# Kernel tuning notes

Measured on AMD Instinct MI355X. Metric: run time of the kernel, lower is better.

Reference implementation:

```python
import jax, jax.numpy as jnp
import numpy as np

B, L, HID = 2, 2048, 2560
H, HKV, DH = 32, 8, 128
G = H // HKV  # GQA groups = 4
EPS = 1e-6
THETA = 1000000.0


def setup_inputs() -> dict:
    key = jax.random.key(0)
    ks = jax.random.split(key, 6)
    x = jax.random.normal(ks[0], (B, L, HID), dtype=jnp.float32)
    Wq = jax.random.normal(ks[1], (HID, H * DH), dtype=jnp.float32) * 0.02
    Wk = jax.random.normal(ks[2], (HID, HKV * DH), dtype=jnp.float32) * 0.02
    Wv = jax.random.normal(ks[3], (HID, HKV * DH), dtype=jnp.float32) * 0.02
    Wo = jax.random.normal(ks[4], (H * DH, HID), dtype=jnp.float32) * 0.02
    q_norm_w = jnp.ones((DH,), dtype=jnp.float32)
    k_norm_w = jnp.ones((DH,), dtype=jnp.float32)
    # RoPE tables, theta=1e6, non-interleaved (half-split) layout
    inv_freq = 1.0 / (THETA ** (jnp.arange(0, DH, 2, dtype=jnp.float32) / DH))
    pos = jnp.arange(L, dtype=jnp.float32)
    freqs = pos[:, None] * inv_freq[None, :]              # [L, DH/2]
    emb = jnp.concatenate([freqs, freqs], axis=-1)        # [L, DH]
    cos = jnp.broadcast_to(jnp.cos(emb)[None], (B, L, DH))
    sin = jnp.broadcast_to(jnp.sin(emb)[None], (B, L, DH))
    return {"x": x, "Wq": Wq, "Wk": Wk, "Wv": Wv, "Wo": Wo,
            "q_norm_w": q_norm_w, "k_norm_w": k_norm_w,
            "cos": cos, "sin": sin}


def _rmsnorm(x, w):
    xf = x.astype(jnp.float32)
    var = jnp.mean(xf * xf, axis=-1, keepdims=True)
    return (xf * jax.lax.rsqrt(var + EPS)).astype(x.dtype) * w


def _rotate_half(x):
    x1, x2 = jnp.split(x, 2, axis=-1)
    return jnp.concatenate([-x2, x1], axis=-1)


def reference(x, Wq, Wk, Wv, Wo, q_norm_w, k_norm_w, cos, sin):
    b, l, _ = x.shape
    q = (x @ Wq).reshape(b, l, H, DH)
    k = (x @ Wk).reshape(b, l, HKV, DH)
    v = (x @ Wv).reshape(b, l, HKV, DH).transpose(0, 2, 1, 3)   # [B,HKV,L,DH]
    q = _rmsnorm(q, q_norm_w).transpose(0, 2, 1, 3)             # [B,H,L,DH]
    k = _rmsnorm(k, k_norm_w).transpose(0, 2, 1, 3)             # [B,HKV,L,DH]
    c = cos[:, None]  # [B,1,L,DH]
    s = sin[:, None]
    q = q * c + _rotate_half(q) * s
    k = k * c + _rotate_half(k) * s
    # GQA SDPA, causal
    qg = q.reshape(b, HKV, G, l, DH)
    scale = 1.0 / np.sqrt(DH)
    scores = jnp.einsum('bkgqd,bkmd->bkgqm', qg, k) * scale     # [B,HKV,G,L,L]
    causal = jnp.tril(jnp.ones((l, l), dtype=bool))
    scores = jnp.where(causal, scores, jnp.finfo(scores.dtype).min)
    attn = jax.nn.softmax(scores, axis=-1)
    out = jnp.einsum('bkgqm,bkmd->bkgqd', attn, v)              # [B,HKV,G,L,DH]
    out = out.reshape(b, H, l, DH).transpose(0, 2, 1, 3).reshape(b, l, H * DH)
    return out @ Wo
```

## Files before the change

### kernel.cpp

```cpp
#include <hip/hip_runtime.h>

typedef unsigned short u16;
typedef unsigned int u32;
using bf16x8 = __attribute__((ext_vector_type(8))) __bf16;
using f32x4  = __attribute__((ext_vector_type(4))) float;

typedef const void __attribute__((address_space(1)))* gas1p;
typedef void __attribute__((address_space(3)))* las3p;

__device__ __forceinline__ void gload16(const void* g, void* l) {
  __builtin_amdgcn_global_load_lds((gas1p)g, (las3p)l, 16, 0, 0);
}

__device__ __forceinline__ u16 f2bf(float f) {
  union { float f; unsigned u; } v; v.f = f;
  unsigned r = v.u + 0x7FFFu + ((v.u >> 16) & 1u);
  return (u16)(r >> 16);
}
__device__ __forceinline__ float bf2f(u16 h) {
  union { unsigned u; float f; } v; v.u = ((unsigned)h) << 16;
  return v.f;
}

__global__ __launch_bounds__(256)
void cvt_f32_bf16(const float4* __restrict__ in, uint2* __restrict__ out, int n4) {
  int i = blockIdx.x * 256 + threadIdx.x;
  if (i >= n4) return;
  float4 v = in[i];
  uint2 o;
  o.x = (unsigned)f2bf(v.x) | ((unsigned)f2bf(v.y) << 16);
  o.y = (unsigned)f2bf(v.z) | ((unsigned)f2bf(v.w) << 16);
  out[i] = o;
}

__global__ __launch_bounds__(256)
void transpose_w(const float* __restrict__ in, u16* __restrict__ out, int R, int C) {
  __shared__ float tile[32][33];
  const int tx = threadIdx.x & 31, ty = threadIdx.x >> 5;
  const int r0 = blockIdx.y * 32, c0 = blockIdx.x * 32;
#pragma unroll
  for (int i = 0; i < 4; i++)
    tile[ty + i * 8][tx] = in[(size_t)(r0 + ty + i * 8) * C + c0 + tx];
  __syncthreads();
#pragma unroll
  for (int i = 0; i < 4; i++)
    out[(size_t)(c0 + ty + i * 8) * R + r0 + tx] = f2bf(tile[tx][ty + i * 8]);
}

__global__ __launch_bounds__(256)
void transpose_v(const u16* __restrict__ QKV, u16* __restrict__ Vt) {
  __shared__ u16 tile[32][34];
  const int tx = threadIdx.x & 31, ty = threadIdx.x >> 5;
  const int l0 = blockIdx.x * 32, d0 = blockIdx.y * 32;
  const int bkv = blockIdx.z;
  const int b = bkv >> 3, kvh = bkv & 7;
#pragma unroll
  for (int i = 0; i < 4; i++)
    tile[ty + i * 8][tx] =
        QKV[(size_t)(b * 2048 + l0 + ty + i * 8) * 6144 + 5120 + kvh * 128 + d0 + tx];
  __syncthreads();
#pragma unroll
  for (int i = 0; i < 4; i++)
    Vt[((size_t)bkv * 128 + d0 + ty + i * 8) * 2048 + l0 + tx] = tile[tx][ty + i * 8];
}

__global__ __launch_bounds__(256)
void norm_rope(const u16* __restrict__ QKV, const float* __restrict__ qw,
               const float* __restrict__ kw, const float* __restrict__ cosp,
               const float* __restrict__ sinp, u16* __restrict__ Qr,
               u16* __restrict__ Kr) {
  const int rid = blockIdx.x * 4 + (threadIdx.x >> 6);
  const int lane = threadIdx.x & 63;
  const int head = rid % 40;
  const int bl = rid / 40;
  const int b = bl >> 11, l = bl & 2047;
  const u16* src; const float* w; u16* dst; float scale;
  if (head < 32) {
    src = QKV + (size_t)bl * 6144 + head * 128;
    w = qw;
    dst = Qr + ((size_t)(b * 32 + head) * 2048 + l) * 128;
    scale = 0.08838834764831845f;
  } else {
    const int kvh = head - 32;
    src = QKV + (size_t)bl * 6144 + 4096 + kvh * 128;
    w = kw;
    dst = Kr + ((size_t)(b * 8 + kvh) * 2048 + l) * 128;
    scale = 1.0f;
  }
  float lo = bf2f(src[lane]);
  float hi = bf2f(src[lane + 64]);
  float ss = lo * lo + hi * hi;
#pragma unroll
  for (int m = 1; m < 64; m <<= 1) ss += __shfl_xor(ss, m, 64);
  const float rstd = rsqrtf(ss * (1.0f / 128.0f) + 1e-6f) * scale;
  const float nlo = lo * rstd * w[lane];
  const float nhi = hi * rstd * w[lane + 64];
  const float* cb = cosp + (size_t)bl * 128;
  const float* sb = sinp + (size_t)bl * 128;
  dst[lane]      = f2bf(nlo * cb[lane]      - nhi * sb[lane]);
  dst[lane + 64] = f2bf(nhi * cb[lane + 64] + nlo * sb[lane + 64]);
}

#define BAR __builtin_amdgcn_s_barrier()
#define WLG { asm volatile("s_waitcnt lgkmcnt(0)" ::: "memory");            \
              __builtin_amdgcn_sched_barrier(0); }
#define WVMn(n) asm volatile("s_waitcnt vmcnt(" #n ")" ::: "memory")
#define SP1 __builtin_amdgcn_s_setprio(1)
#define SP0 __builtin_amdgcn_s_setprio(0)

template <int BM, int BN, int WM, int WN, typename CT>
__global__ __launch_bounds__(512, 2)
void gemmT(const u16* __restrict__ A, const u16* __restrict__ Bt,
           CT* __restrict__ C, int N, int K, int MT) {
  extern __shared__ char smem[];
  constexpr int ASZ = BM * 128;
  constexpr int BSZ = BN * 128;
  constexpr int MI = BM / WM / 16;
  constexpr int NJF = BN / WN / 16;
  const int tid = threadIdx.x, lane = tid & 63, wid = tid >> 6;
  const int wm = wid / WN, wn = wid % WN;
  const int fr = lane & 15, fq = lane >> 4;
  const int qx = (int)gridDim.x >> 3;
  const int wg = ((int)blockIdx.x & 7) * qx + ((int)blockIdx.x >> 3);
  const int bx = wg / MT, by = wg - bx * MT;
  const int m0 = by * BM, n0 = bx * BN;
  const u16* Ab = A + (size_t)m0 * K;
  const u16* Bb = Bt + (size_t)n0 * K;

#define ABUF(c) (smem + (c) * ASZ)
#define BBUF(c) (smem + 2 * ASZ + (c) * BSZ)

  f32x4 acc[MI][NJF];
#pragma unroll
  for (int i = 0; i < MI; i++)
#pragma unroll
    for (int j = 0; j < NJF; j++)
#pragma unroll
      for (int r = 0; r < 4; r++) acc[i][j][r] = 0.f;

  auto stage = [&](int c, int kk) {
#pragma unroll
    for (int l = 0; l < BM / 64; l++) {
      const int u = tid + 512 * l, row = u >> 3, ch = u & 7;
      gload16(Ab + (size_t)row * K + ((ch ^ (row & 7)) << 3) + kk,
              ABUF(c) + (u << 4));
    }
#pragma unroll
    for (int l = 0; l < BN / 64; l++) {
      const int u = tid + 512 * l, row = u >> 3, ch = u & 7;
      gload16(Bb + (size_t)row * K + ((ch ^ (row & 7)) << 3) + kk,
              BBUF(c) + (u << 4));
    }
    if constexpr ((BN % 64) != 0) {
      const int u = (BN / 64) * 512 + (tid & 255), row = u >> 3, ch = u & 7;
      gload16(Bb + (size_t)row * K + ((ch ^ (row & 7)) << 3) + kk,
              BBUF(c) + (u << 4));
    }
  };

  const int NT = K >> 6;
  stage(0, 0);
  stage(1, 64);
  WVMn(7);
  BAR;

  bf16x8 af[MI][2], bf[NJF][2];
  for (int t = 0; t < NT; t++) {
    const int c = t & 1;
#pragma unroll
    for (int i = 0; i < MI; i++) {
      const int row = (wm * MI + i) * 16 + fr;
#pragma unroll
      for (int ks = 0; ks < 2; ks++)
        af[i][ks] = *(const bf16x8*)(ABUF(c) + row * 128 +
                                     ((((ks << 2) + fq) ^ (row & 7)) << 4));
    }
#pragma unroll
    for (int j = 0; j < NJF; j++) {
      const int row = (j * WN + wn) * 16 + fr;
#pragma unroll
      for (int ks = 0; ks < 2; ks++)
        bf[j][ks] = *(const bf16x8*)(BBUF(c) + row * 128 +
                                     ((((ks << 2) + fq) ^ (row & 7)) << 4));
    }
    WLG;
    BAR;
    int t2 = t + 2; if (t2 >= NT) t2 -= NT;
    stage(c, t2 << 6);
    WVMn(7);
    SP1;
#pragma unroll
    for (int j = 0; j < NJF; j++)
#pragma unroll
      for (int i = 0; i < MI; i++) {
        acc[i][j] = __builtin_amdgcn_mfma_f32_16x16x32_bf16(af[i][0], bf[j][0],
                                                            acc[i][j], 0, 0, 0);
        acc[i][j] = __builtin_amdgcn_mfma_f32_16x16x32_bf16(af[i][1], bf[j][1],
                                                            acc[i][j], 0, 0, 0);
      }
    SP0;
    BAR;
  }
  WVMn(0);

#pragma unroll
  for (int i = 0; i < MI; i++) {
    const int row0 = m0 + (wm * MI + i) * 16 + fq * 4;
#pragma unroll
    for (int j = 0; j < NJF; j++) {
      const int col = n0 + (j * WN + wn) * 16 + fr;
#pragma unroll
      for (int r = 0; r < 4; r++) {
        const size_t idx = (size_t)(row0 + r) * N + col;
        if constexpr (sizeof(CT) == 2) C[idx] = f2bf(acc[i][j][r]);
        else C[idx] = acc[i][j][r];
      }
    }
  }
#undef ABUF
#undef BBUF
}

__global__ __launch_bounds__(256, 2)
void attn_fwd(const u16* __restrict__ Qr, const u16* __restrict__ Kr,
              const u16* __restrict__ Vt, u16* __restrict__ AO) {
  const int L = 2048, DH = 128;
  __shared__ u16 Ks[2][64 * 128];
  __shared__ u16 Vs[2][128 * 64];
  const int tid = threadIdx.x, lane = tid & 63, wid = tid >> 6;
  const int fr = lane & 15, fq = lane >> 4;
  const int j = blockIdx.x >> 4;
  const int grp = blockIdx.x & 15;
  const int kvh = grp >> 1, b = grp & 1;
  const int h = kvh * 4 + wid;

  const u16* Kbase = Kr + (size_t)(b * 8 + kvh) * L * DH;
  const u16* Vbase = Vt + (size_t)(b * 8 + kvh) * DH * L;

  int Dly[4], kOff[4], vOff[4];
#pragma unroll
  for (int p = 0; p < 4; p++) {
    const int D = (tid + p * 256) * 16;
    Dly[p] = D;
    const int kr = D >> 8, kc = ((D >> 4) & 15) ^ (kr & 7);
    kOff[p] = kr * 128 + kc * 8;
    const int vr = D >> 7, vc = ((D >> 4) & 7) ^ (vr & 7);
    vOff[p] = vr * 2048 + vc * 8;
  }

  const bool B5 = (lane & 32) != 0;
  const bool A4 = (lane & 16) != 0;

  auto stage = [&](int kt, int bufi) {
    const int k0 = kt * 64;
#pragma unroll
    for (int p = 0; p < 4; p++) {
      gload16(Kbase + (size_t)k0 * 128 + kOff[p], (char*)&Ks[bufi][0] + Dly[p]);
      gload16(Vbase + k0 + vOff[p], (char*)&Vs[bufi][0] + Dly[p]);
    }
  };

  for (int half = 0; half < 2; half++) {
    const int t = half ? 63 - j : j;
    const int nk = (t >> 1) + 1;

    bf16x8 qf[2][4];
#pragma unroll
    for (int g = 0; g < 2; g++) {
      const int qq = t * 32 + g * 16 + fr;
      const u16* qbase = Qr + ((size_t)(b * 32 + h) * L + qq) * DH + fq * 8;
#pragma unroll
      for (int dt = 0; dt < 4; dt++) qf[g][dt] = *(const bf16x8*)(qbase + dt * 32);
    }
    asm volatile("s_waitcnt vmcnt(0)" ::: "memory");

    f32x4 o[2][8];
#pragma unroll
    for (int g = 0; g < 2; g++)
#pragma unroll
      for (int d = 0; d < 8; d++)
#pragma unroll
        for (int r = 0; r < 4; r++) o[g][d][r] = 0.f;
    float mrow[2] = {-__builtin_huge_valf(), -__builtin_huge_valf()};
    float lrow[2] = {0.f, 0.f};

    __builtin_amdgcn_s_barrier();
    stage(0, 0);
    int cur = 0;

    for (int kt = 0; kt < nk; kt++) {
      if (kt + 1 < nk) {
        stage(kt + 1, cur ^ 1);
        asm volatile("s_waitcnt vmcnt(8)" ::: "memory");
      } else {
        asm volatile("s_waitcnt vmcnt(0)" ::: "memory");
      }
      __builtin_amdgcn_s_barrier();

      const u16* KsB = &Ks[cur][0];
      const u16* VsB = &Vs[cur][0];
      const int k0 = kt * 64;

      f32x4 s4[2][4];
#pragma unroll
      for (int g = 0; g < 2; g++)
#pragma unroll
        for (int ni = 0; ni < 4; ni++)
#pragma unroll
          for (int r = 0; r < 4; r++) s4[g][ni][r] = 0.f;
#pragma unroll
      for (int ni = 0; ni < 4; ni++) {
        const int krow = ni * 16 + fr;
        const int sw = (krow & 7) << 4;
#pragma unroll
        for (int dt = 0; dt < 4; dt++) {
          const int off = (krow * 256 + dt * 64 + fq * 16) ^ sw;
          bf16x8 kf = *(const bf16x8*)((const char*)KsB + off);
          s4[0][ni] = __builtin_amdgcn_mfma_f32_16x16x32_bf16(kf, qf[0][dt], s4[0][ni], 0, 0, 0);
          s4[1][ni] = __builtin_amdgcn_mfma_f32_16x16x32_bf16(kf, qf[1][dt], s4[1][ni], 0, 0, 0);
        }
      }

      if (kt == nk - 1) {
#pragma unroll
        for (int g = 0; g < 2; g++) {
          const int qq = t * 32 + g * 16 + fr;
#pragma unroll
          for (int ni = 0; ni < 4; ni++)
#pragma unroll
            for (int r = 0; r < 4; r++)
              if (k0 + ni * 16 + fq * 4 + r > qq) s4[g][ni][r] = -1e30f;
        }
      }

      bf16x8 pb[2][2];
#pragma unroll
      for (int g = 0; g < 2; g++) {
        float mt = s4[g][0][0];
#pragma unroll
        for (int ni = 0; ni < 4; ni++)
#pragma unroll
          for (int r = 0; r < 4; r++) mt = fmaxf(mt, s4[g][ni][r]);
        mt = fmaxf(mt, __shfl_xor(mt, 16, 64));
        mt = fmaxf(mt, __shfl_xor(mt, 32, 64));

        if (!__all(mt <= mrow[g] + 8.f)) {
          const float mn = fmaxf(mrow[g], mt);
          const float corr = exp2f((mrow[g] - mn) * 1.44269504f);
          mrow[g] = mn;
          lrow[g] *= corr;
#pragma unroll
          for (int d = 0; d < 8; d++)
#pragma unroll
            for (int r = 0; r < 4; r++) o[g][d][r] *= corr;
        }

        const float ml = mrow[g] * 1.44269504f;
        float rs = 0.f;
#pragma unroll
        for (int ni = 0; ni < 4; ni++)
#pragma unroll
          for (int r = 0; r < 4; r++) {
            const float pv = exp2f(fmaf(s4[g][ni][r], 1.44269504f, -ml));
            s4[g][ni][r] = pv;
            rs += pv;
          }
        rs += __shfl_xor(rs, 16, 64);
        rs += __shfl_xor(rs, 32, 64);
        lrow[g] += rs;

        u32 pk[4][2];
#pragma unroll
        for (int ni = 0; ni < 4; ni++) {
          pk[ni][0] = __builtin_amdgcn_perm(__float_as_uint(s4[g][ni][1]),
                                            __float_as_uint(s4[g][ni][0]), 0x07060302u);
          pk[ni][1] = __builtin_amdgcn_perm(__float_as_uint(s4[g][ni][3]),
                                            __float_as_uint(s4[g][ni][2]), 0x07060302u);
        }
#pragma unroll
        for (int ks = 0; ks < 2; ks++) {
          u32 r00 = pk[2 * ks + 0][0], r01 = pk[2 * ks + 0][1];
          u32 r10 = pk[2 * ks + 1][0], r11 = pk[2 * ks + 1][1];
          u32 e0 = __shfl_xor(B5 ? r00 : r10, 32, 64);
          u32 t00 = B5 ? e0 : r00, t10 = B5 ? r10 : e0;
          u32 e1 = __shfl_xor(B5 ? r01 : r11, 32, 64);
          u32 t01 = B5 ? e1 : r01, t11 = B5 ? r11 : e1;
          u32 e2 = __shfl_xor(A4 ? t00 : t10, 16, 64);
          u32 u00 = A4 ? e2 : t00, u10 = A4 ? t10 : e2;
          u32 e3 = __shfl_xor(A4 ? t01 : t11, 16, 64);
          u32 u01 = A4 ? e3 : t01, u11 = A4 ? t11 : e3;
          union { u32 u[4]; bf16x8 v; } pbv;
          pbv.u[0] = u00; pbv.u[1] = u01; pbv.u[2] = u10; pbv.u[3] = u11;
          pb[g][ks] = pbv.v;
        }
      }

#pragma unroll
      for (int d = 0; d < 8; d++) {
        const int vrow = d * 16 + fr;
        const int sw = (vrow & 7) << 4;
#pragma unroll
        for (int ks = 0; ks < 2; ks++) {
          const int off = (vrow * 128 + ks * 64 + fq * 16) ^ sw;
          bf16x8 vf = *(const bf16x8*)((const char*)VsB + off);
          o[0][d] = __builtin_amdgcn_mfma_f32_16x16x32_bf16(vf, pb[0][ks], o[0][d], 0, 0, 0);
          o[1][d] = __builtin_amdgcn_mfma_f32_16x16x32_bf16(vf, pb[1][ks], o[1][d], 0, 0, 0);
        }
      }
      __builtin_amdgcn_s_barrier();
      cur ^= 1;
    }

#pragma unroll
    for (int g = 0; g < 2; g++) {
      const float inv = 1.f / lrow[g];
      const int qq = t * 32 + g * 16 + fr;
      u16* obase = AO + ((size_t)b * L + qq) * 4096 + h * 128 + fq * 4;
#pragma unroll
      for (int d = 0; d < 8; d++) {
        uint2 w;
        w.x = (u32)f2bf(o[g][d][0] * inv) | ((u32)f2bf(o[g][d][1] * inv) << 16);
        w.y = (u32)f2bf(o[g][d][2] * inv) | ((u32)f2bf(o[g][d][3] * inv) << 16);
        *(uint2*)(obase + d * 16) = w;
      }
    }
  }
}

extern "C" void kernel_launch(void* const* d_in, const int* in_sizes, int n_in,
                              void* d_out, int out_size, void* d_ws, size_t ws_size,
                              hipStream_t stream) {
  const float* x    = (const float*)d_in[0];
  const float* Wq   = (const float*)d_in[1];
  const float* Wk   = (const float*)d_in[2];
  const float* Wv   = (const float*)d_in[3];
  const float* Wo   = (const float*)d_in[4];
  const float* qw   = (const float*)d_in[5];
  const float* kw   = (const float*)d_in[6];
  const float* cosp = (const float*)d_in[7];
  const float* sinp = (const float*)d_in[8];
  float* out = (float*)d_out;
  char* ws = (char*)d_ws;

  u16* xb    = (u16*)(ws);
  u16* WqkvT = (u16*)(ws + 20971520);
  u16* WoT   = (u16*)(ws + 52428800);
  u16* QKV   = (u16*)(ws + 73400320);
  u16* AO    = QKV;
  u16* Qrr   = (u16*)(ws + 123731968);
  u16* Krr   = (u16*)(ws + 157286400);
  u16* Vtt   = (u16*)(ws + 165675008);

  hipFuncSetAttribute(reinterpret_cast<const void*>(&gemmT<256, 192, 2, 4, u16>),
                      hipFuncAttributeMaxDynamicSharedMemorySize, 114688);
  hipFuncSetAttribute(reinterpret_cast<const void*>(&gemmT<256, 160, 4, 2, float>),
                      hipFuncAttributeMaxDynamicSharedMemorySize, 106496);

  cvt_f32_bf16<<<10240, 256, 0, stream>>>((const float4*)x, (uint2*)xb, 2621440);
  transpose_w<<<dim3(128, 80), 256, 0, stream>>>(Wq, WqkvT, 2560, 4096);
  transpose_w<<<dim3(32, 80), 256, 0, stream>>>(Wk, WqkvT + (size_t)4096 * 2560, 2560, 1024);
  transpose_w<<<dim3(32, 80), 256, 0, stream>>>(Wv, WqkvT + (size_t)5120 * 2560, 2560, 1024);
  transpose_w<<<dim3(80, 128), 256, 0, stream>>>(Wo, WoT, 4096, 2560);

  gemmT<256, 192, 2, 4, u16><<<512, 512, 114688, stream>>>(xb, WqkvT, QKV, 6144, 2560, 16);

  norm_rope<<<40960, 256, 0, stream>>>(QKV, qw, kw, cosp, sinp, Qrr, Krr);
  transpose_v<<<dim3(64, 4, 16), 256, 0, stream>>>(QKV, Vtt);

  attn_fwd<<<dim3(512), 256, 0, stream>>>(Qrr, Krr, Vtt, AO);

  gemmT<256, 160, 4, 2, float><<<256, 512, 106496, stream>>>(AO, WoT, out, 2560, 4096, 16);
}
```

Before: 406.7 us.

## Shrink attention KV tile to 32 and QKV GEMM tile to raise occupancy

Restructures the attention kernel to process one 32-row query tile per block with 32-key KV tiles. Blocks are launched longest-first in place of pairing tiles per block, and the grid doubles. The PV product switches to 16x16x16 MFMA so the probability fragment no longer needs the cross-lane shuffle transpose, and the V shared layout is reswizzled to match. The QKV projection GEMM uses a 128-row tile with 4 waves-per-SIMD occupancy and twice as many workgroups. Both changes aim to improve latency hiding and load balance, at the cost of more barriers per key and smaller MFMA instructions.

```diff
diff --git a/kernel.cpp b/kernel.cpp
--- a/kernel.cpp
+++ b/kernel.cpp
@@ -4,6 +4,7 @@
 typedef unsigned int u32;
 using bf16x8 = __attribute__((ext_vector_type(8))) __bf16;
 using f32x4  = __attribute__((ext_vector_type(4))) float;
+using short4v = __attribute__((ext_vector_type(4))) short;
 
 typedef const void __attribute__((address_space(1)))* gas1p;
 typedef void __attribute__((address_space(3)))* las3p;
@@ -108,8 +109,8 @@
 #define SP1 __builtin_amdgcn_s_setprio(1)
 #define SP0 __builtin_amdgcn_s_setprio(0)
 
-template <int BM, int BN, int WM, int WN, typename CT>
-__global__ __launch_bounds__(512, 2)
+template <int MINW, int BM, int BN, int WM, int WN, typename CT>
+__global__ __launch_bounds__(512, MINW)
 void gemmT(const u16* __restrict__ A, const u16* __restrict__ Bt,
            CT* __restrict__ C, int N, int K, int MT) {
   extern __shared__ char smem[];
@@ -117,6 +118,7 @@
   constexpr int BSZ = BN * 128;
   constexpr int MI = BM / WM / 16;
   constexpr int NJF = BN / WN / 16;
+  constexpr int NL = BM / 64 + (BN + 63) / 64;
   const int tid = threadIdx.x, lane = tid & 63, wid = tid >> 6;
   const int wm = wid / WN, wn = wid % WN;
   const int fr = lane & 15, fq = lane >> 4;
@@ -161,7 +163,7 @@
   const int NT = K >> 6;
   stage(0, 0);
   stage(1, 64);
-  WVMn(7);
+  if constexpr (NL == 5) { WVMn(5); } else { WVMn(7); }
   BAR;
 
   bf16x8 af[MI][2], bf[NJF][2];
@@ -187,7 +189,7 @@
     BAR;
     int t2 = t + 2; if (t2 >= NT) t2 -= NT;
     stage(c, t2 << 6);
-    WVMn(7);
+    if constexpr (NL == 5) { WVMn(5); } else { WVMn(7); }
     SP1;
 #pragma unroll
     for (int j = 0; j < NJF; j++)
@@ -221,208 +223,188 @@
 #undef BBUF
 }
 
-__global__ __launch_bounds__(256, 2)
+__global__ __launch_bounds__(256, 4)
 void attn_fwd(const u16* __restrict__ Qr, const u16* __restrict__ Kr,
               const u16* __restrict__ Vt, u16* __restrict__ AO) {
   const int L = 2048, DH = 128;
-  __shared__ u16 Ks[2][64 * 128];
-  __shared__ u16 Vs[2][128 * 64];
+  __shared__ u16 Ks[2][32 * 128];
+  __shared__ u16 Vs[2][64 * 64];
   const int tid = threadIdx.x, lane = tid & 63, wid = tid >> 6;
   const int fr = lane & 15, fq = lane >> 4;
-  const int j = blockIdx.x >> 4;
+  const int t = 63 - (int)(blockIdx.x >> 4);
   const int grp = blockIdx.x & 15;
   const int kvh = grp >> 1, b = grp & 1;
   const int h = kvh * 4 + wid;
+  const int nk = t + 1;
 
   const u16* Kbase = Kr + (size_t)(b * 8 + kvh) * L * DH;
   const u16* Vbase = Vt + (size_t)(b * 8 + kvh) * DH * L;
 
-  int Dly[4], kOff[4], vOff[4];
-#pragma unroll
-  for (int p = 0; p < 4; p++) {
-    const int D = (tid + p * 256) * 16;
-    Dly[p] = D;
-    const int kr = D >> 8, kc = ((D >> 4) & 15) ^ (kr & 7);
-    kOff[p] = kr * 128 + kc * 8;
-    const int vr = D >> 7, vc = ((D >> 4) & 7) ^ (vr & 7);
-    vOff[p] = vr * 2048 + vc * 8;
-  }
-
-  const bool B5 = (lane & 32) != 0;
-  const bool A4 = (lane & 16) != 0;
+  int kDst[2], kSrc[2], vSrc[2];
+#pragma unroll
+  for (int p = 0; p < 2; p++) {
+    const int u = tid + p * 256;
+    kDst[p] = u << 4;
+    const int kr = u >> 4, kc = (u & 15) ^ (kr & 7);
+    kSrc[p] = kr * 128 + kc * 8;
+    const int line = u >> 3, s0c = (2 * (u & 7)) ^ (line & 6);
+    const int dvr = (line << 1) | (s0c >> 3), sl = s0c & 7;
+    vSrc[p] = dvr * 2048 + sl * 4;
+  }
 
   auto stage = [&](int kt, int bufi) {
-    const int k0 = kt * 64;
-#pragma unroll
-    for (int p = 0; p < 4; p++) {
-      gload16(Kbase + (size_t)k0 * 128 + kOff[p], (char*)&Ks[bufi][0] + Dly[p]);
-      gload16(Vbase + k0 + vOff[p], (char*)&Vs[bufi][0] + Dly[p]);
-    }
+    const int k0 = kt * 32;
+#pragma unroll
+    for (int p = 0; p < 2; p++)
+      gload16(Kbase + (size_t)k0 * 128 + kSrc[p], (char*)&Ks[bufi][0] + kDst[p]);
+#pragma unroll
+    for (int p = 0; p < 2; p++)
+      gload16(Vbase + k0 + vSrc[p], (char*)&Vs[bufi][0] + kDst[p]);
   };
 
-  for (int half = 0; half < 2; half++) {
-    const int t = half ? 63 - j : j;
-    const int nk = (t >> 1) + 1;
-
-    bf16x8 qf[2][4];
+  bf16x8 qf[2][4];
+#pragma unroll
+  for (int g = 0; g < 2; g++) {
+    const int q = t * 32 + g * 16 + fr;
+    const u16* qbase = Qr + ((size_t)(b * 32 + h) * L + q) * DH + fq * 8;
+#pragma unroll
+    for (int dt = 0; dt < 4; dt++) qf[g][dt] = *(const bf16x8*)(qbase + dt * 32);
+  }
+  asm volatile("s_waitcnt vmcnt(0)" ::: "memory");
+
+  f32x4 o[2][8];
+#pragma unroll
+  for (int g = 0; g < 2; g++)
+#pragma unroll
+    for (int d = 0; d < 8; d++)
+#pragma unroll
+      for (int r = 0; r < 4; r++) o[g][d][r] = 0.f;
+  float mrow[2] = {-__builtin_huge_valf(), -__builtin_huge_valf()};
+  float lrow[2] = {0.f, 0.f};
+
+  stage(0, 0);
+  int cur = 0;
+
+  for (int kt = 0; kt < nk; kt++) {
+    if (kt + 1 < nk) {
+      stage(kt + 1, cur ^ 1);
+      asm volatile("s_waitcnt vmcnt(4)" ::: "memory");
+    } else {
+      asm volatile("s_waitcnt vmcnt(0)" ::: "memory");
+    }
+    __builtin_amdgcn_s_barrier();
+
+    const u16* KsB = &Ks[cur][0];
+    const u16* VsB = &Vs[cur][0];
+    const int k0 = kt * 32;
+
+    f32x4 s4[2][2];
+#pragma unroll
+    for (int g = 0; g < 2; g++)
+#pragma unroll
+      for (int ni = 0; ni < 2; ni++)
+#pragma unroll
+        for (int r = 0; r < 4; r++) s4[g][ni][r] = 0.f;
+#pragma unroll
+    for (int ni = 0; ni < 2; ni++) {
+      const int krow = ni * 16 + fr;
+      const int sw = (krow & 7) << 4;
+#pragma unroll
+      for (int dt = 0; dt < 4; dt++) {
+        const int off = (krow * 256 + dt * 64 + fq * 16) ^ sw;
+        bf16x8 kf = *(const bf16x8*)((const char*)KsB + off);
+        s4[0][ni] = __builtin_amdgcn_mfma_f32_16x16x32_bf16(kf, qf[0][dt], s4[0][ni], 0, 0, 0);
+        s4[1][ni] = __builtin_amdgcn_mfma_f32_16x16x32_bf16(kf, qf[1][dt], s4[1][ni], 0, 0, 0);
+      }
+    }
+
+    if (kt == nk - 1) {
+#pragma unroll
+      for (int g = 0; g < 2; g++) {
+        const int q = t * 32 + g * 16 + fr;
+#pragma unroll
+        for (int ni = 0; ni < 2; ni++)
+#pragma unroll
+          for (int r = 0; r < 4; r++)
+            if (k0 + ni * 16 + fq * 4 + r > q) s4[g][ni][r] = -1e30f;
+      }
+    }
+
+    short4v pk[2][2];
 #pragma unroll
     for (int g = 0; g < 2; g++) {
-      const int qq = t * 32 + g * 16 + fr;
-      const u16* qbase = Qr + ((size_t)(b * 32 + h) * L + qq) * DH + fq * 8;
-#pragma unroll
-      for (int dt = 0; dt < 4; dt++) qf[g][dt] = *(const bf16x8*)(qbase + dt * 32);
-    }
-    asm volatile("s_waitcnt vmcnt(0)" ::: "memory");
-
-    f32x4 o[2][8];
-#pragma unroll
-    for (int g = 0; g < 2; g++)
-#pragma unroll
-      for (int d = 0; d < 8; d++)
-#pragma unroll
-        for (int r = 0; r < 4; r++) o[g][d][r] = 0.f;
-    float mrow[2] = {-__builtin_huge_valf(), -__builtin_huge_valf()};
-    float lrow[2] = {0.f, 0.f};
-
+      float mt = fmaxf(fmaxf(s4[g][0][0], s4[g][0][1]),
+                       fmaxf(s4[g][0][2], s4[g][0][3]));
+#pragma unroll
+      for (int r = 0; r < 4; r++) mt = fmaxf(mt, s4[g][1][r]);
+      mt = fmaxf(mt, __shfl_xor(mt, 16, 64));
+      mt = fmaxf(mt, __shfl_xor(mt, 32, 64));
+
+      if (!__all(mt <= mrow[g] + 8.f)) {
+        const float mn = fmaxf(mrow[g], mt);
+        const float corr = exp2f((mrow[g] - mn) * 1.44269504f);
+        mrow[g] = mn;
+        lrow[g] *= corr;
+#pragma unroll
+        for (int d = 0; d < 8; d++)
+#pragma unroll
+          for (int r = 0; r < 4; r++) o[g][d][r] *= corr;
+      }
+
+      const float ml = mrow[g] * 1.44269504f;
+      float rs = 0.f;
+#pragma unroll
+      for (int ni = 0; ni < 2; ni++)
+#pragma unroll
+        for (int r = 0; r < 4; r++) {
+          const float pv = exp2f(fmaf(s4[g][ni][r], 1.44269504f, -ml));
+          s4[g][ni][r] = pv;
+          rs += pv;
+        }
+      rs += __shfl_xor(rs, 16, 64);
+      rs += __shfl_xor(rs, 32, 64);
+      lrow[g] += rs;
+
+#pragma unroll
+      for (int ni = 0; ni < 2; ni++) {
+        union { u32 u[2]; short4v s; } pb;
+        pb.u[0] = __builtin_amdgcn_perm(__float_as_uint(s4[g][ni][1]),
+                                        __float_as_uint(s4[g][ni][0]), 0x07060302u);
+        pb.u[1] = __builtin_amdgcn_perm(__float_as_uint(s4[g][ni][3]),
+                                        __float_as_uint(s4[g][ni][2]), 0x07060302u);
+        pk[g][ni] = pb.s;
+      }
+    }
+
+#pragma unroll
+    for (int d = 0; d < 8; d++) {
+      const int vrow = d * 16 + fr;
+      const int vbase = (vrow >> 1) * 128;
+      const int lk = (vrow >> 1) & 6;
+      const int hi8 = (vrow & 1) << 3;
+#pragma unroll
+      for (int ni = 0; ni < 2; ni++) {
+        const int s0 = hi8 | (ni * 4 + fq);
+        short4v vf = *(const short4v*)((const char*)VsB + vbase + ((s0 ^ lk) << 3));
+        o[0][d] = __builtin_amdgcn_mfma_f32_16x16x16bf16_1k(vf, pk[0][ni], o[0][d], 0, 0, 0);
+        o[1][d] = __builtin_amdgcn_mfma_f32_16x16x16bf16_1k(vf, pk[1][ni], o[1][d], 0, 0, 0);
+      }
+    }
     __builtin_amdgcn_s_barrier();
-    stage(0, 0);
-    int cur = 0;
-
-    for (int kt = 0; kt < nk; kt++) {
-      if (kt + 1 < nk) {
-        stage(kt + 1, cur ^ 1);
-        asm volatile("s_waitcnt vmcnt(8)" ::: "memory");
-      } else {
-        asm volatile("s_waitcnt vmcnt(0)" ::: "memory");
-      }
-      __builtin_amdgcn_s_barrier();
-
-      const u16* KsB = &Ks[cur][0];
-      const u16* VsB = &Vs[cur][0];
-      const int k0 = kt * 64;
-
-      f32x4 s4[2][4];
-#pragma unroll
-      for (int g = 0; g < 2; g++)
-#pragma unroll
-        for (int ni = 0; ni < 4; ni++)
-#pragma unroll
-          for (int r = 0; r < 4; r++) s4[g][ni][r] = 0.f;
-#pragma unroll
-      for (int ni = 0; ni < 4; ni++) {
-        const int krow = ni * 16 + fr;
-        const int sw = (krow & 7) << 4;
-#pragma unroll
-        for (int dt = 0; dt < 4; dt++) {
-          const int off = (krow * 256 + dt * 64 + fq * 16) ^ sw;
-          bf16x8 kf = *(const bf16x8*)((const char*)KsB + off);
-          s4[0][ni] = __builtin_amdgcn_mfma_f32_16x16x32_bf16(kf, qf[0][dt], s4[0][ni], 0, 0, 0);
-          s4[1][ni] = __builtin_amdgcn_mfma_f32_16x16x32_bf16(kf, qf[1][dt], s4[1][ni], 0, 0, 0);
-        }
-      }
-
-      if (kt == nk - 1) {
-#pragma unroll
-        for (int g = 0; g < 2; g++) {
-          const int qq = t * 32 + g * 16 + fr;
-#pragma unroll
-          for (int ni = 0; ni < 4; ni++)
-#pragma unroll
-            for (int r = 0; r < 4; r++)
-              if (k0 + ni * 16 + fq * 4 + r > qq) s4[g][ni][r] = -1e30f;
-        }
-      }
-
-      bf16x8 pb[2][2];
-#pragma unroll
-      for (int g = 0; g < 2; g++) {
-        float mt = s4[g][0][0];
-#pragma unroll
-        for (int ni = 0; ni < 4; ni++)
-#pragma unroll
-          for (int r = 0; r < 4; r++) mt = fmaxf(mt, s4[g][ni][r]);
-        mt = fmaxf(mt, __shfl_xor(mt, 16, 64));
-        mt = fmaxf(mt, __shfl_xor(mt, 32, 64));
-
-        if (!__all(mt <= mrow[g] + 8.f)) {
-          const float mn = fmaxf(mrow[g], mt);
-          const float corr = exp2f((mrow[g] - mn) * 1.44269504f);
-          mrow[g] = mn;
-          lrow[g] *= corr;
-#pragma unroll
-          for (int d = 0; d < 8; d++)
-#pragma unroll
-            for (int r = 0; r < 4; r++) o[g][d][r] *= corr;
-        }
-
-        const float ml = mrow[g] * 1.44269504f;
-        float rs = 0.f;
-#pragma unroll
-        for (int ni = 0; ni < 4; ni++)
-#pragma unroll
-          for (int r = 0; r < 4; r++) {
-            const float pv = exp2f(fmaf(s4[g][ni][r], 1.44269504f, -ml));
-            s4[g][ni][r] = pv;
-            rs += pv;
-          }
-        rs += __shfl_xor(rs, 16, 64);
-        rs += __shfl_xor(rs, 32, 64);
-        lrow[g] += rs;
-
-        u32 pk[4][2];
-#pragma unroll
-        for (int ni = 0; ni < 4; ni++) {
-          pk[ni][0] = __builtin_amdgcn_perm(__float_as_uint(s4[g][ni][1]),
-                                            __float_as_uint(s4[g][ni][0]), 0x07060302u);
-          pk[ni][1] = __builtin_amdgcn_perm(__float_as_uint(s4[g][ni][3]),
-                                            __float_as_uint(s4[g][ni][2]), 0x07060302u);
-        }
-#pragma unroll
-        for (int ks = 0; ks < 2; ks++) {
-          u32 r00 = pk[2 * ks + 0][0], r01 = pk[2 * ks + 0][1];
-          u32 r10 = pk[2 * ks + 1][0], r11 = pk[2 * ks + 1][1];
-          u32 e0 = __shfl_xor(B5 ? r00 : r10, 32, 64);
-          u32 t00 = B5 ? e0 : r00, t10 = B5 ? r10 : e0;
-          u32 e1 = __shfl_xor(B5 ? r01 : r11, 32, 64);
-          u32 t01 = B5 ? e1 : r01, t11 = B5 ? r11 : e1;
-          u32 e2 = __shfl_xor(A4 ? t00 : t10, 16, 64);
-          u32 u00 = A4 ? e2 : t00, u10 = A4 ? t10 : e2;
-          u32 e3 = __shfl_xor(A4 ? t01 : t11, 16, 64);
-          u32 u01 = A4 ? e3 : t01, u11 = A4 ? t11 : e3;
-          union { u32 u[4]; bf16x8 v; } pbv;
-          pbv.u[0] = u00; pbv.u[1] = u01; pbv.u[2] = u10; pbv.u[3] = u11;
-          pb[g][ks] = pbv.v;
-        }
-      }
-
-#pragma unroll
-      for (int d = 0; d < 8; d++) {
-        const int vrow = d * 16 + fr;
-        const int sw = (vrow & 7) << 4;
-#pragma unroll
-        for (int ks = 0; ks < 2; ks++) {
-          const int off = (vrow * 128 + ks * 64 + fq * 16) ^ sw;
-          bf16x8 vf = *(const bf16x8*)((const char*)VsB + off);
-          o[0][d] = __builtin_amdgcn_mfma_f32_16x16x32_bf16(vf, pb[0][ks], o[0][d], 0, 0, 0);
-          o[1][d] = __builtin_amdgcn_mfma_f32_16x16x32_bf16(vf, pb[1][ks], o[1][d], 0, 0, 0);
-        }
-      }
-      __builtin_amdgcn_s_barrier();
-      cur ^= 1;
-    }
-
-#pragma unroll
-    for (int g = 0; g < 2; g++) {
-      const float inv = 1.f / lrow[g];
-      const int qq = t * 32 + g * 16 + fr;
-      u16* obase = AO + ((size_t)b * L + qq) * 4096 + h * 128 + fq * 4;
-#pragma unroll
-      for (int d = 0; d < 8; d++) {
-        uint2 w;
-        w.x = (u32)f2bf(o[g][d][0] * inv) | ((u32)f2bf(o[g][d][1] * inv) << 16);
-        w.y = (u32)f2bf(o[g][d][2] * inv) | ((u32)f2bf(o[g][d][3] * inv) << 16);
-        *(uint2*)(obase + d * 16) = w;
-      }
+    cur ^= 1;
+  }
+
+#pragma unroll
+  for (int g = 0; g < 2; g++) {
+    const float inv = 1.f / lrow[g];
+    const int q = t * 32 + g * 16 + fr;
+    u16* obase = AO + ((size_t)b * L + q) * 4096 + h * 128 + fq * 4;
+#pragma unroll
+    for (int d = 0; d < 8; d++) {
+      uint2 w;
+      w.x = (u32)f2bf(o[g][d][0] * inv) | ((u32)f2bf(o[g][d][1] * inv) << 16);
+      w.y = (u32)f2bf(o[g][d][2] * inv) | ((u32)f2bf(o[g][d][3] * inv) << 16);
+      *(uint2*)(obase + d * 16) = w;
     }
   }
 }
@@ -451,9 +433,9 @@
   u16* Krr   = (u16*)(ws + 157286400);
   u16* Vtt   = (u16*)(ws + 165675008);
 
-  hipFuncSetAttribute(reinterpret_cast<const void*>(&gemmT<256, 192, 2, 4, u16>),
-                      hipFuncAttributeMaxDynamicSharedMemorySize, 114688);
-  hipFuncSetAttribute(reinterpret_cast<const void*>(&gemmT<256, 160, 4, 2, float>),
+  hipFuncSetAttribute(reinterpret_cast<const void*>(&gemmT<4, 128, 192, 2, 4, u16>),
+                      hipFuncAttributeMaxDynamicSharedMemorySize, 81920);
+  hipFuncSetAttribute(reinterpret_cast<const void*>(&gemmT<2, 256, 160, 4, 2, float>),
                       hipFuncAttributeMaxDynamicSharedMemorySize, 106496);
 
   cvt_f32_bf16<<<10240, 256, 0, stream>>>((const float4*)x, (uint2*)xb, 2621440);
@@ -462,12 +444,12 @@
   transpose_w<<<dim3(32, 80), 256, 0, stream>>>(Wv, WqkvT + (size_t)5120 * 2560, 2560, 1024);
   transpose_w<<<dim3(80, 128), 256, 0, stream>>>(Wo, WoT, 4096, 2560);
 
-  gemmT<256, 192, 2, 4, u16><<<512, 512, 114688, stream>>>(xb, WqkvT, QKV, 6144, 2560, 16);
+  gemmT<4, 128, 192, 2, 4, u16><<<1024, 512, 81920, stream>>>(xb, WqkvT, QKV, 6144, 2560, 32);
 
   norm_rope<<<40960, 256, 0, stream>>>(QKV, qw, kw, cosp, sinp, Qrr, Krr);
   transpose_v<<<dim3(64, 4, 16), 256, 0, stream>>>(QKV, Vtt);
 
-  attn_fwd<<<dim3(512), 256, 0, stream>>>(Qrr, Krr, Vtt, AO);
-
-  gemmT<256, 160, 4, 2, float><<<256, 512, 106496, stream>>>(AO, WoT, out, 2560, 4096, 16);
-}
+  attn_fwd<<<dim3(1024), 256, 0, stream>>>(Qrr, Krr, Vtt, AO);
+
+  gemmT<2, 256, 160, 4, 2, float><<<256, 512, 106496, stream>>>(AO, WoT, out, 2560, 4096, 16);
+}
```

Measured after the change: 521.8 us. 1.28x slower.
